# Optimization experiments

Measured on AMD Instinct MI355X. Metric: run time of the kernel, lower is better.

The kernel has to match this reference:

```python
import jax, jax.numpy as jnp
from jax import lax
import numpy as np

B, C, H, W = 32, 32, 64, 64
HD = 128          # hidden_dim per direction
OUT = 128         # output_dim
IN_DIM = 2 * HD + C   # linear input: [x, h_up, h_left]


def setup_inputs() -> dict:
    key = jax.random.key(0)
    ks = jax.random.split(key, 10)
    x = jax.random.normal(ks[0], (B, C, H, W), dtype=jnp.float32)
    # 4 directional MDLSTM cells, params stacked on leading dim
    lin_scale = 1.0 / np.sqrt(IN_DIM)
    W_lin = jax.random.normal(ks[1], (4, 5 * HD, IN_DIM), dtype=jnp.float32) * lin_scale
    b_lin = jax.random.normal(ks[2], (4, 5 * HD), dtype=jnp.float32) * lin_scale
    # peephole weights: torch uses uniform_(0,1); scale down for numeric stability
    Wci = jax.random.uniform(ks[3], (4, 1, HD), dtype=jnp.float32) * 0.1
    Wf1 = jax.random.uniform(ks[4], (4, 1, HD), dtype=jnp.float32) * 0.1
    Wf2 = jax.random.uniform(ks[5], (4, 1, HD), dtype=jnp.float32) * 0.1
    Wco = jax.random.uniform(ks[6], (4, 1, HD), dtype=jnp.float32) * 0.1
    # 1x1 conv: weight [OUT, 4*HD]
    W_conv = jax.random.normal(ks[7], (OUT, 4 * HD), dtype=jnp.float32) / np.sqrt(4 * HD)
    b_conv = jax.random.normal(ks[8], (OUT,), dtype=jnp.float32) * 0.01
    return {"x": x, "W_lin": W_lin, "b_lin": b_lin, "Wci": Wci, "Wf1": Wf1,
            "Wf2": Wf2, "Wco": Wco, "W_conv": W_conv, "b_conv": b_conv}


def _mdlstm_scan(x, Wl, bl, wci, wf1, wf2, wco):
    # x: [H, W, B, C] -> h: [H, W, B, HD].
    # Recurrence: (i,j) depends on (i-1,j) (up) and (i,j-1) (left), zero at borders
    # (clamped-index reads in the torch code hit still-zero h/c entries).
    Wdim, Bb = x.shape[1], x.shape[2]
    zeros = jnp.zeros((Bb, HD), x.dtype)

    def col_step(carry, inp):
        h_left, c_left = carry
        x_ij, h_up, c_up = inp                       # [B,C], [B,HD], [B,HD]
        z = jnp.concatenate([x_ij, h_up, h_left], axis=1) @ Wl.T + bl  # [B,5HD]
        i_g, f1, f2, g, o = jnp.split(z, 5, axis=1)
        i_g = jax.nn.sigmoid(i_g + wci * c_up + wci * c_left)
        f1 = jax.nn.sigmoid(f1 + wf1 * c_up)
        f2 = jax.nn.sigmoid(f2 + wf2 * c_left)
        c_next = f1 * c_up + f2 * c_left + i_g * jnp.tanh(g)
        o = jax.nn.sigmoid(o + wco * c_next)
        h_next = o * jnp.tanh(c_next)
        return (h_next, c_next), (h_next, c_next)

    def row_step(carry, x_row):
        h_up_row, c_up_row = carry                   # [W, B, HD]
        _, (h_row, c_row) = lax.scan(col_step, (zeros, zeros),
                                     (x_row, h_up_row, c_up_row))
        return (h_row, c_row), h_row

    row_init = (jnp.zeros((Wdim, Bb, HD), x.dtype),
                jnp.zeros((Wdim, Bb, HD), x.dtype))
    _, h_all = lax.scan(row_step, row_init, x)       # [H, W, B, HD]
    return h_all


# direction flips, matching torch order: hf_vf, hr_vf (flip H), hf_vr (flip W), hr_vr
_FLIPS = [(False, False), (True, False), (False, True), (True, True)]


def reference(x, W_lin, b_lin, Wci, Wf1, Wf2, Wco, W_conv, b_conv):
    xp = jnp.transpose(x, (2, 3, 0, 1))              # [H, W, B, C]
    outs = []
    for d, (f0, f1) in enumerate(_FLIPS):
        xi = xp
        if f0:
            xi = xi[::-1]
        if f1:
            xi = xi[:, ::-1]
        # NOTE: original code does NOT flip outputs back before concatenating.
        outs.append(_mdlstm_scan(xi, W_lin[d], b_lin[d], Wci[d], Wf1[d], Wf2[d], Wco[d]))
    comb = jnp.concatenate(outs, axis=3)             # [H, W, B, 4*HD]
    out = jnp.einsum('hwbc,oc->bohw', comb, W_conv) + b_conv[None, :, None, None]
    return out                                       # [B, OUT, H, W]
```

## Files before the change

kernel.cpp:

```cpp
#include <hip/hip_runtime.h>
#include <hip/hip_bf16.h>


#define HDIM 128
#define ZDIM 640
#define KDIM 288

__device__ __forceinline__ float sigmoidf_(float v) {
    return 1.0f / (1.0f + __expf(-v));
}
__device__ __forceinline__ float tanhf_(float v) {
    return 1.0f - 2.0f / (__expf(2.0f * v) + 1.0f);
}

__global__ void transpose_weights(const float* __restrict__ W_lin,
                                  const float* __restrict__ W_conv,
                                  float* __restrict__ Wt,
                                  float* __restrict__ Wct) {
    int idx = blockIdx.x * 256 + threadIdx.x;
    const int NLIN = 4 * ZDIM * KDIM;
    if (idx < NLIN) {
        int d = idx / (ZDIM * KDIM);
        int r = idx % (ZDIM * KDIM);
        int col = r / KDIM;
        int k = r % KDIM;
        Wt[d * (ZDIM * KDIM) + k * ZDIM + col] = W_lin[idx];
    } else {
        int idx2 = idx - NLIN;
        if (idx2 < 128 * 512) {
            int o = idx2 / 512, c = idx2 % 512;
            Wct[c * 128 + o] = W_conv[idx2];
        }
    }
}

__global__ __launch_bounds__(256) void transpose_x(const float* __restrict__ x,
                                                   float* __restrict__ x_t) {
    __shared__ float tile[64][65];
    int tb = blockIdx.x >> 6;
    int tj = blockIdx.x & 63;
    int t = threadIdx.x;
    for (int f = t; f < 4096; f += 256) {
        int r = f >> 6, cix = f & 63;
        tile[r][cix] = x[(size_t)(tb * 64 + r) * 4096 + tj * 64 + cix];
    }
    __syncthreads();
    for (int f = t; f < 4096; f += 256) {
        int rr = f >> 6, cc = f & 63;
        x_t[(size_t)(tj * 64 + rr) * 1024 + tb * 64 + cc] = tile[cc][rr];
    }
}

__global__ void fill_sentinel(float* __restrict__ out) {
    out[blockIdx.x * 256 + threadIdx.x] = 1.0e6f;
}

__global__ __launch_bounds__(256) void fused_step(
    const float* __restrict__ x_t,
    const float* __restrict__ Wt,
    const float* __restrict__ b_lin,
    const float* __restrict__ Wci, const float* __restrict__ Wf1,
    const float* __restrict__ Wf2, const float* __restrict__ Wco,
    const float* __restrict__ Wct,
    const float* __restrict__ b_conv,
    float* __restrict__ h_par,
    float* __restrict__ c_par,
    float* __restrict__ out,
    int s, int i0, int nc, int i0p, int ncp, int nstep) {
    __shared__ __align__(16) float smem[8 * 512];

    const int t = threadIdx.x;
    const int blk = blockIdx.x;
    const int par = s & 1, parR = par ^ 1;

    if (blk < nstep) {
        int hf = blk & 1;
        int r = blk >> 1;
        int bt = r & 3;
        r >>= 2;
        int ci = r % nc;
        int d = r / nc;
        int i = i0 + ci, j = s - i;
        int fi = (d & 1) ? 63 - i : i;
        int fj = (d & 2) ? 63 - j : j;

        {
            int bb = t >> 5, c = t & 31;
            smem[bb * KDIM + c] =
                x_t[(size_t)(fi * 64 + fj) * 1024 + (bt * 8 + bb) * 32 + c];
        }
        {
            const float* hu =
                (i > 0) ? h_par + (((size_t)(parR * 4 + d) * 64 + (i - 1)) * 32 +
                                   bt * 8) * HDIM
                        : nullptr;
            const float* hl =
                (j > 0) ? h_par + (((size_t)(parR * 4 + d) * 64 + i) * 32 +
                                   bt * 8) * HDIM
                        : nullptr;
            int bb = t >> 5, k4 = t & 31;
            float4 z4 = make_float4(0.f, 0.f, 0.f, 0.f);
            float4 vu = hu ? ((const float4*)hu)[t] : z4;
            float4 vl = hl ? ((const float4*)hl)[t] : z4;
            *(float4*)&smem[bb * KDIM + 32 + k4 * 4] = vu;
            *(float4*)&smem[bb * KDIM + 160 + k4 * 4] = vl;
        }
        __syncthreads();

        const int lane = t & 63, w = t >> 6;
        const int cb = hf * 64 + lane;
        const float* wp = Wt + (size_t)d * (KDIM * ZDIM) + cb;
        const float* xr0 = smem + (w * 2 + 0) * KDIM;
        const float* xr1 = smem + (w * 2 + 1) * KDIM;

        float acc[5][2];
#pragma unroll
        for (int g = 0; g < 5; ++g) {
            float bv = b_lin[d * ZDIM + g * 128 + cb];
            acc[g][0] = bv;
            acc[g][1] = bv;
        }
#pragma unroll 4
        for (int kk = 0; kk < KDIM; ++kk) {
            const float* wr = wp + (size_t)kk * ZDIM;
            float x0 = xr0[kk], x1 = xr1[kk];
#pragma unroll
            for (int g = 0; g < 5; ++g) {
                float wv = wr[g * 128];
                acc[g][0] = fmaf(wv, x0, acc[g][0]);
                acc[g][1] = fmaf(wv, x1, acc[g][1]);
            }
        }

        const float wciv = Wci[d * HDIM + cb];
        const float wf1v = Wf1[d * HDIM + cb];
        const float wf2v = Wf2[d * HDIM + cb];
        const float wcov = Wco[d * HDIM + cb];
        size_t wbase = ((size_t)(par * 4 + d) * 64 + i) * 32 * HDIM;
        float* cw = c_par + wbase;
        float* hw = h_par + wbase;
        const float* cu_b =
            (i > 0) ? c_par + ((size_t)(parR * 4 + d) * 64 + (i - 1)) * 32 * HDIM
                    : nullptr;
        const float* cl_b =
            (j > 0) ? c_par + ((size_t)(parR * 4 + d) * 64 + i) * 32 * HDIM
                    : nullptr;
#pragma unroll
        for (int p = 0; p < 2; ++p) {
            int b = bt * 8 + w * 2 + p;
            float cu = cu_b ? cu_b[b * HDIM + cb] : 0.f;
            float cl = cl_b ? cl_b[b * HDIM + cb] : 0.f;
            float ig = sigmoidf_(acc[0][p] + wciv * (cu + cl));
            float f1 = sigmoidf_(acc[1][p] + wf1v * cu);
            float f2 = sigmoidf_(acc[2][p] + wf2v * cl);
            float cn = f1 * cu + f2 * cl + ig * tanhf_(acc[3][p]);
            float oo = sigmoidf_(acc[4][p] + wcov * cn);
            float hn = oo * tanhf_(cn);
            cw[b * HDIM + cb] = cn;
            hw[b * HDIM + cb] = hn;
        }
    } else {
        int cb2 = blk - nstep;
        int btc = cb2 & 3, cip = cb2 >> 2;
        int ip = i0p + cip, jp = (s - 1) - ip;

        for (int f = t; f < 1024; f += 256) {
            int d = f >> 8, rem = f & 255;
            int bb = rem >> 5, k4 = rem & 31;
            const float4* src =
                (const float4*)(h_par + (((size_t)(parR * 4 + d) * 64 + ip) * 32 +
                                         btc * 8 + bb) * HDIM);
            *(float4*)&smem[bb * 512 + d * 128 + k4 * 4] = src[k4];
        }
        __syncthreads();

        const int o = t & 127, half = t >> 7;
        float acc[4];
#pragma unroll
        for (int q = 0; q < 4; ++q) acc[q] = b_conv[o];
#pragma unroll 4
        for (int c = 0; c < 512; ++c) {
            float wv = Wct[c * 128 + o];
#pragma unroll
            for (int q = 0; q < 4; ++q)
                acc[q] = fmaf(smem[(half * 4 + q) * 512 + c], wv, acc[q]);
        }
#pragma unroll
        for (int q = 0; q < 4; ++q) {
            int b = btc * 8 + half * 4 + q;
            out[(size_t)(b * 128 + o) * 4096 + ip * 64 + jp] = acc[q];
        }
    }
}

extern "C" void kernel_launch(void* const* d_in, const int* in_sizes, int n_in,
                              void* d_out, int out_size, void* d_ws,
                              size_t ws_size, hipStream_t stream) {
    const float* x = (const float*)d_in[0];
    const float* W_lin = (const float*)d_in[1];
    const float* b_lin = (const float*)d_in[2];
    const float* Wci = (const float*)d_in[3];
    const float* Wf1 = (const float*)d_in[4];
    const float* Wf2 = (const float*)d_in[5];
    const float* Wco = (const float*)d_in[6];
    const float* W_conv = (const float*)d_in[7];
    const float* b_conv = (const float*)d_in[8];
    float* out = (float*)d_out;

    const size_t N_HPAR = 2ull * 4 * 64 * 32 * 128;
    const size_t N_WT = 4ull * KDIM * ZDIM;
    const size_t N_WCT = 512ull * 128;
    const size_t N_XT = 4096ull * 1024;
    float* h_par = (float*)d_ws;
    float* c_par = h_par + N_HPAR;
    float* Wt = c_par + N_HPAR;
    float* Wct = Wt + N_WT;
    float* x_t = Wct + N_WCT;
    size_t need = (2 * N_HPAR + N_WT + N_WCT + N_XT) * 4ull;
    if (ws_size < need) {
        fill_sentinel<<<(out_size + 255) / 256, 256, 0, stream>>>(out);
        return;
    }

    transpose_weights<<<3136, 256, 0, stream>>>(W_lin, W_conv, Wt, Wct);
    transpose_x<<<1024, 256, 0, stream>>>(x, x_t);

    for (int s = 0; s <= 127; ++s) {
        int i0 = 0, nc = 0;
        if (s <= 126) {
            i0 = s > 63 ? s - 63 : 0;
            int i1 = s < 63 ? s : 63;
            nc = i1 - i0 + 1;
        }
        int i0p = 0, ncp = 0;
        if (s >= 1) {
            int sp = s - 1;
            i0p = sp > 63 ? sp - 63 : 0;
            int i1p = sp < 63 ? sp : 63;
            ncp = i1p - i0p + 1;
        }
        int nstep = 32 * nc;
        int nconv = 4 * ncp;
        fused_step<<<nstep + nconv, 256, 0, stream>>>(
            x_t, Wt, b_lin, Wci, Wf1, Wf2, Wco, Wct, b_conv, h_par, c_par, out,
            s, i0, nc, i0p, ncp, nstep);
    }
}
```

Measured before the change: 7.666 ms.

## Register-tile the LSTM gate GEMM over 64 rows per block

Each step block now processes two diagonal cells times all 32 batch rows (64 rows) against 64 hidden columns, with each thread holding an 8x2x5 accumulator tile. Every weight load is reused across 8 rows instead of 2, and the weight matrix is read by far fewer blocks. The aim is to cut redundant global weight traffic. In exchange there are fewer blocks per launch, large register pressure from 80 accumulators, and a 73KB shared buffer that limits occupancy.

```diff
diff --git a/kernel.cpp b/kernel.cpp
--- a/kernel.cpp
+++ b/kernel.cpp
@@ -13,18 +13,17 @@
     return 1.0f - 2.0f / (__expf(2.0f * v) + 1.0f);
 }
 
-__global__ void transpose_weights(const float* __restrict__ W_lin,
-                                  const float* __restrict__ W_conv,
-                                  float* __restrict__ Wt,
-                                  float* __restrict__ Wct) {
+__global__ void prep_weights(const float* __restrict__ W_lin,
+                             const float* __restrict__ W_conv,
+                             float* __restrict__ Wt, float* __restrict__ Wct) {
     int idx = blockIdx.x * 256 + threadIdx.x;
     const int NLIN = 4 * ZDIM * KDIM;
     if (idx < NLIN) {
         int d = idx / (ZDIM * KDIM);
         int r = idx % (ZDIM * KDIM);
-        int col = r / KDIM;
+        int n = r / KDIM;
         int k = r % KDIM;
-        Wt[d * (ZDIM * KDIM) + k * ZDIM + col] = W_lin[idx];
+        Wt[d * (ZDIM * KDIM) + k * ZDIM + n] = W_lin[idx];
     } else {
         int idx2 = idx - NLIN;
         if (idx2 < 128 * 512) {
@@ -66,111 +65,149 @@
     float* __restrict__ h_par,
     float* __restrict__ c_par,
     float* __restrict__ out,
-    int s, int i0, int nc, int i0p, int ncp, int nstep) {
-    __shared__ __align__(16) float smem[8 * 512];
+    int s, int i0, int nc, int mt, int i0p, int ncp, int nstep) {
+    __shared__ __align__(16) float smem[64 * KDIM];
 
     const int t = threadIdx.x;
     const int blk = blockIdx.x;
     const int par = s & 1, parR = par ^ 1;
 
     if (blk < nstep) {
-        int hf = blk & 1;
-        int r = blk >> 1;
-        int bt = r & 3;
-        r >>= 2;
-        int ci = r % nc;
-        int d = r / nc;
-        int i = i0 + ci, j = s - i;
-        int fi = (d & 1) ? 63 - i : i;
-        int fj = (d & 2) ? 63 - j : j;
-
-        {
-            int bb = t >> 5, c = t & 31;
-            smem[bb * KDIM + c] =
-                x_t[(size_t)(fi * 64 + fj) * 1024 + (bt * 8 + bb) * 32 + c];
-        }
-        {
-            const float* hu =
-                (i > 0) ? h_par + (((size_t)(parR * 4 + d) * 64 + (i - 1)) * 32 +
-                                   bt * 8) * HDIM
-                        : nullptr;
-            const float* hl =
-                (j > 0) ? h_par + (((size_t)(parR * 4 + d) * 64 + i) * 32 +
-                                   bt * 8) * HDIM
-                        : nullptr;
-            int bb = t >> 5, k4 = t & 31;
-            float4 z4 = make_float4(0.f, 0.f, 0.f, 0.f);
-            float4 vu = hu ? ((const float4*)hu)[t] : z4;
-            float4 vl = hl ? ((const float4*)hl)[t] : z4;
-            *(float4*)&smem[bb * KDIM + 32 + k4 * 4] = vu;
-            *(float4*)&smem[bb * KDIM + 160 + k4 * 4] = vl;
+        int r0 = blk;
+        const int cbt = r0 & 1;
+        r0 >>= 1;
+        const int mtile = r0 % mt;
+        const int d = r0 / mt;
+
+        const size_t slotR = (size_t)(parR * 4 + d) * 64;
+        const size_t slotW = (size_t)(par * 4 + d) * 64;
+
+        int ivec[2], jvec[2], ijf[2];
+        bool val[2];
+#pragma unroll
+        for (int cs = 0; cs < 2; ++cs) {
+            int ct = mtile * 2 + cs;
+            val[cs] = ct < nc;
+            int i = i0 + ct, j = s - i;
+            ivec[cs] = i;
+            jvec[cs] = j;
+            int fi = (d & 1) ? 63 - i : i;
+            int fj = (d & 2) ? 63 - j : j;
+            ijf[cs] = fi * 64 + fj;
+        }
+
+        for (int f = t; f < 512; f += 256) {
+            int row = f >> 3, k4 = f & 7;
+            int cs = row >> 5, b = row & 31;
+            float4 v = make_float4(0.f, 0.f, 0.f, 0.f);
+            if (val[cs])
+                v = *(const float4*)(x_t + (size_t)ijf[cs] * 1024 + b * 32 +
+                                     k4 * 4);
+            *(float4*)&smem[row * KDIM + k4 * 4] = v;
+        }
+        for (int f = t; f < 2048; f += 256) {
+            int row = f >> 5, k4 = f & 31;
+            int cs = row >> 5, b = row & 31;
+            float4 v = make_float4(0.f, 0.f, 0.f, 0.f);
+            if (val[cs] && ivec[cs] > 0)
+                v = *(const float4*)(h_par +
+                                     (slotR + (size_t)(ivec[cs] - 1)) * 4096 +
+                                     b * 128 + k4 * 4);
+            *(float4*)&smem[row * KDIM + 32 + k4 * 4] = v;
+        }
+        for (int f = t; f < 2048; f += 256) {
+            int row = f >> 5, k4 = f & 31;
+            int cs = row >> 5, b = row & 31;
+            float4 v = make_float4(0.f, 0.f, 0.f, 0.f);
+            if (val[cs] && jvec[cs] > 0)
+                v = *(const float4*)(h_par + (slotR + (size_t)ivec[cs]) * 4096 +
+                                     b * 128 + k4 * 4);
+            *(float4*)&smem[row * KDIM + 160 + k4 * 4] = v;
         }
         __syncthreads();
 
-        const int lane = t & 63, w = t >> 6;
-        const int cb = hf * 64 + lane;
-        const float* wp = Wt + (size_t)d * (KDIM * ZDIM) + cb;
-        const float* xr0 = smem + (w * 2 + 0) * KDIM;
-        const float* xr1 = smem + (w * 2 + 1) * KDIM;
-
-        float acc[5][2];
+        const int rg = t >> 5;
+        const int c2 = t & 31;
+        const int cb0 = cbt * 64 + c2 * 2;
+        const float* wbase = Wt + (size_t)d * (KDIM * ZDIM);
+        const float* xrow = smem + (rg * 8) * KDIM;
+
+        float acc[8][2][5];
 #pragma unroll
         for (int g = 0; g < 5; ++g) {
-            float bv = b_lin[d * ZDIM + g * 128 + cb];
-            acc[g][0] = bv;
-            acc[g][1] = bv;
-        }
-#pragma unroll 4
-        for (int kk = 0; kk < KDIM; ++kk) {
-            const float* wr = wp + (size_t)kk * ZDIM;
-            float x0 = xr0[kk], x1 = xr1[kk];
+#pragma unroll
+            for (int cc = 0; cc < 2; ++cc) {
+                float bv = b_lin[d * ZDIM + g * 128 + cb0 + cc];
+#pragma unroll
+                for (int rr = 0; rr < 8; ++rr) acc[rr][cc][g] = bv;
+            }
+        }
+
+#pragma unroll 2
+        for (int k = 0; k < KDIM; ++k) {
+            float xv[8];
+#pragma unroll
+            for (int rr = 0; rr < 8; ++rr) xv[rr] = xrow[rr * KDIM + k];
+            const float* wk = wbase + (size_t)k * ZDIM + cb0;
+            float wv[2][5];
 #pragma unroll
             for (int g = 0; g < 5; ++g) {
-                float wv = wr[g * 128];
-                acc[g][0] = fmaf(wv, x0, acc[g][0]);
-                acc[g][1] = fmaf(wv, x1, acc[g][1]);
+                float2 w2 = *(const float2*)(wk + g * 128);
+                wv[0][g] = w2.x;
+                wv[1][g] = w2.y;
             }
-        }
-
-        const float wciv = Wci[d * HDIM + cb];
-        const float wf1v = Wf1[d * HDIM + cb];
-        const float wf2v = Wf2[d * HDIM + cb];
-        const float wcov = Wco[d * HDIM + cb];
-        size_t wbase = ((size_t)(par * 4 + d) * 64 + i) * 32 * HDIM;
-        float* cw = c_par + wbase;
-        float* hw = h_par + wbase;
-        const float* cu_b =
-            (i > 0) ? c_par + ((size_t)(parR * 4 + d) * 64 + (i - 1)) * 32 * HDIM
-                    : nullptr;
-        const float* cl_b =
-            (j > 0) ? c_par + ((size_t)(parR * 4 + d) * 64 + i) * 32 * HDIM
-                    : nullptr;
-#pragma unroll
-        for (int p = 0; p < 2; ++p) {
-            int b = bt * 8 + w * 2 + p;
-            float cu = cu_b ? cu_b[b * HDIM + cb] : 0.f;
-            float cl = cl_b ? cl_b[b * HDIM + cb] : 0.f;
-            float ig = sigmoidf_(acc[0][p] + wciv * (cu + cl));
-            float f1 = sigmoidf_(acc[1][p] + wf1v * cu);
-            float f2 = sigmoidf_(acc[2][p] + wf2v * cl);
-            float cn = f1 * cu + f2 * cl + ig * tanhf_(acc[3][p]);
-            float oo = sigmoidf_(acc[4][p] + wcov * cn);
-            float hn = oo * tanhf_(cn);
-            cw[b * HDIM + cb] = cn;
-            hw[b * HDIM + cb] = hn;
+#pragma unroll
+            for (int rr = 0; rr < 8; ++rr)
+#pragma unroll
+                for (int cc = 0; cc < 2; ++cc)
+#pragma unroll
+                    for (int g = 0; g < 5; ++g)
+                        acc[rr][cc][g] =
+                            fmaf(xv[rr], wv[cc][g], acc[rr][cc][g]);
+        }
+
+        const int cs = rg >> 2;
+        if (val[cs]) {
+            const int i = ivec[cs], j = jvec[cs];
+            const size_t ru = (slotR + (size_t)(i - 1)) * 4096;
+            const size_t rl = (slotR + (size_t)i) * 4096;
+            const size_t wbase2 = (slotW + (size_t)i) * 4096;
+#pragma unroll
+            for (int cc = 0; cc < 2; ++cc) {
+                int col = cb0 + cc;
+                float wciv = Wci[d * HDIM + col];
+                float wf1v = Wf1[d * HDIM + col];
+                float wf2v = Wf2[d * HDIM + col];
+                float wcov = Wco[d * HDIM + col];
+#pragma unroll
+                for (int rr = 0; rr < 8; ++rr) {
+                    int b = (rg * 8 + rr) & 31;
+                    float cu = (i > 0) ? c_par[ru + b * 128 + col] : 0.f;
+                    float cl = (j > 0) ? c_par[rl + b * 128 + col] : 0.f;
+                    float ig = sigmoidf_(acc[rr][cc][0] + wciv * (cu + cl));
+                    float f1 = sigmoidf_(acc[rr][cc][1] + wf1v * cu);
+                    float f2 = sigmoidf_(acc[rr][cc][2] + wf2v * cl);
+                    float cn = f1 * cu + f2 * cl + ig * tanhf_(acc[rr][cc][3]);
+                    float oo = sigmoidf_(acc[rr][cc][4] + wcov * cn);
+                    float hn = oo * tanhf_(cn);
+                    c_par[wbase2 + b * 128 + col] = cn;
+                    h_par[wbase2 + b * 128 + col] = hn;
+                }
+            }
         }
     } else {
         int cb2 = blk - nstep;
         int btc = cb2 & 3, cip = cb2 >> 2;
         int ip = i0p + cip, jp = (s - 1) - ip;
+        float* hs = smem;
 
         for (int f = t; f < 1024; f += 256) {
-            int d = f >> 8, rem = f & 255;
+            int dd = f >> 8, rem = f & 255;
             int bb = rem >> 5, k4 = rem & 31;
-            const float4* src =
-                (const float4*)(h_par + (((size_t)(parR * 4 + d) * 64 + ip) * 32 +
-                                         btc * 8 + bb) * HDIM);
-            *(float4*)&smem[bb * 512 + d * 128 + k4 * 4] = src[k4];
+            float4 v = *(const float4*)(
+                h_par + ((size_t)(parR * 4 + dd) * 64 + ip) * 4096 +
+                (btc * 8 + bb) * 128 + k4 * 4);
+            *(float4*)&hs[bb * 512 + dd * 128 + k4 * 4] = v;
         }
         __syncthreads();
 
@@ -183,7 +220,7 @@
             float wv = Wct[c * 128 + o];
 #pragma unroll
             for (int q = 0; q < 4; ++q)
-                acc[q] = fmaf(smem[(half * 4 + q) * 512 + c], wv, acc[q]);
+                acc[q] = fmaf(hs[(half * 4 + q) * 512 + c], wv, acc[q]);
         }
 #pragma unroll
         for (int q = 0; q < 4; ++q) {
@@ -207,30 +244,31 @@
     const float* b_conv = (const float*)d_in[8];
     float* out = (float*)d_out;
 
-    const size_t N_HPAR = 2ull * 4 * 64 * 32 * 128;
+    const size_t N_PAR = 2ull * 4 * 64 * 32 * 128;
     const size_t N_WT = 4ull * KDIM * ZDIM;
     const size_t N_WCT = 512ull * 128;
     const size_t N_XT = 4096ull * 1024;
     float* h_par = (float*)d_ws;
-    float* c_par = h_par + N_HPAR;
-    float* Wt = c_par + N_HPAR;
+    float* c_par = h_par + N_PAR;
+    float* Wt = c_par + N_PAR;
     float* Wct = Wt + N_WT;
     float* x_t = Wct + N_WCT;
-    size_t need = (2 * N_HPAR + N_WT + N_WCT + N_XT) * 4ull;
+    size_t need = (2 * N_PAR + N_WT + N_WCT + N_XT) * 4ull;
     if (ws_size < need) {
         fill_sentinel<<<(out_size + 255) / 256, 256, 0, stream>>>(out);
         return;
     }
 
-    transpose_weights<<<3136, 256, 0, stream>>>(W_lin, W_conv, Wt, Wct);
+    prep_weights<<<3136, 256, 0, stream>>>(W_lin, W_conv, Wt, Wct);
     transpose_x<<<1024, 256, 0, stream>>>(x, x_t);
 
     for (int s = 0; s <= 127; ++s) {
-        int i0 = 0, nc = 0;
+        int i0 = 0, nc = 0, mt = 1;
         if (s <= 126) {
             i0 = s > 63 ? s - 63 : 0;
             int i1 = s < 63 ? s : 63;
             nc = i1 - i0 + 1;
+            mt = (nc + 1) / 2;
         }
         int i0p = 0, ncp = 0;
         if (s >= 1) {
@@ -239,10 +277,10 @@
             int i1p = sp < 63 ? sp : 63;
             ncp = i1p - i0p + 1;
         }
-        int nstep = 32 * nc;
+        int nstep = (s <= 126) ? 4 * mt * 2 : 0;
         int nconv = 4 * ncp;
         fused_step<<<nstep + nconv, 256, 0, stream>>>(
             x_t, Wt, b_lin, Wci, Wf1, Wf2, Wco, Wct, b_conv, h_par, c_par, out,
-            s, i0, nc, i0p, ncp, nstep);
-    }
-}
+            s, i0, nc, mt, i0p, ncp, nstep);
+    }
+}
```

After: 10.45 ms. 1.36x slower.
